# Kernel optimization log

Hardware: AMD Instinct MI355X
Metric: run time of the kernel (lower is better)

Reference implementation:

```python
import jax, jax.numpy as jnp
import numpy as np
import math

B, N, C_IN = 4, 512, 32
K = 3            # Chebyshev order -> K+1 polynomial terms
H = 4            # attention heads
OUT_PER_HEAD = 64
ACT_OUT = OUT_PER_HEAD * H  # concat_heads=True


def _prelu(x, a):
    return jnp.where(x >= 0, x, a * x)


def setup_inputs() -> dict:
    key = jax.random.key(0)
    ks = jax.random.split(key, 10)
    stdv = 1.0 / math.sqrt(ACT_OUT)
    inp = {
        "X_real": jax.random.normal(ks[0], (B, N, C_IN), jnp.float32),
        "X_imag": jax.random.normal(ks[1], (B, N, C_IN), jnp.float32),
        "L_real": jax.random.normal(ks[2], (B, K + 1, N, N), jnp.float32),
        "L_imag": jax.random.normal(ks[3], (B, K + 1, N, N), jnp.float32),
        # Chebyshev complex weights, uniform(-stdv, stdv) as in torch init
        "weight_real": jax.random.uniform(ks[4], (K + 1, C_IN, ACT_OUT), jnp.float32, -stdv, stdv),
        "weight_imag": jax.random.uniform(ks[5], (K + 1, C_IN, ACT_OUT), jnp.float32, -stdv, stdv),
        # CVLinear(2*C_IN -> H) complex weight/bias
        "attn_w_real": jax.random.normal(ks[6], (2 * C_IN, H), jnp.float32) * 0.1,
        "attn_w_imag": jax.random.normal(ks[7], (2 * C_IN, H), jnp.float32) * 0.1,
        "attn_b_real": jnp.zeros((H,), jnp.float32),
        "attn_b_imag": jnp.zeros((H,), jnp.float32),
        # CPReLU slopes (PReLU applied to real/imag parts independently)
        "prelu_a_real": jnp.float32(0.25),
        "prelu_a_imag": jnp.float32(0.25),
        "bias_real": jnp.zeros((1, ACT_OUT), jnp.float32),
        "bias_imag": jnp.zeros((1, ACT_OUT), jnp.float32),
    }
    return inp


def reference(X_real, X_imag, L_real, L_imag, weight_real, weight_imag,
              attn_w_real, attn_w_imag, attn_b_real, attn_b_imag,
              prelu_a_real, prelu_a_imag, bias_real, bias_imag):
    C = X_real.shape[-1]
    K1 = weight_real.shape[0]
    # --- attention scores: complex linear on concat([X_i, X_j]) ---
    # split the 2C weight into the X_i half and the X_j half (same math,
    # avoids materializing the B*N*N*2C pairwise concat tensor)
    W1r, W2r = attn_w_real[:C], attn_w_real[C:]
    W1i, W2i = attn_w_imag[:C], attn_w_imag[C:]
    si_re = X_real @ W1r - X_imag @ W1i   # (B,N,H)
    si_im = X_real @ W1i + X_imag @ W1r
    sj_re = X_real @ W2r - X_imag @ W2i
    sj_im = X_real @ W2i + X_imag @ W2r
    # scores[b,i,j,h]
    sc_re = si_re[:, :, None, :] + sj_re[:, None, :, :] + attn_b_real
    sc_im = si_im[:, :, None, :] + sj_im[:, None, :, :] + attn_b_imag
    # CPReLU: PReLU on real/imag independently
    sc_re = _prelu(sc_re, prelu_a_real)
    sc_im = _prelu(sc_im, prelu_a_imag)
    # adjacency mask from |L_real| summed over the K+1 polynomial terms
    mask = (jnp.abs(L_real).sum(axis=1) > 1e-9)[..., None]  # (B,N,N,1)
    NEG = jnp.float32(-1e9)
    re_m = jnp.where(mask, sc_re, NEG)
    im_m = jnp.where(mask, sc_im, NEG)
    attn = jax.nn.softmax(re_m * re_m + im_m * im_m, axis=2)  # softmax over j, (B,N,N,H)
    # --- complex Chebyshev propagation: (L*attn) @ X, per k, per head ---
    lre_xr = jnp.einsum('bknj,bnjh,bjc->bknch', L_real, attn, X_real)
    lim_xi = jnp.einsum('bknj,bnjh,bjc->bknch', L_imag, attn, X_imag)
    lre_xi = jnp.einsum('bknj,bnjh,bjc->bknch', L_real, attn, X_imag)
    lim_xr = jnp.einsum('bknj,bnjh,bjc->bknch', L_imag, attn, X_real)
    LXr = lre_xr - lim_xi
    LXi = lre_xi + lim_xr
    # per-head complex weights: (K+1, C, P, H), out index = p*H + h
    Wr = weight_real.reshape(K1, C, OUT_PER_HEAD, H)
    Wi = weight_imag.reshape(K1, C, OUT_PER_HEAD, H)
    Yre = jnp.einsum('bknch,kcph->bnph', LXr, Wr) - jnp.einsum('bknch,kcph->bnph', LXi, Wi)
    Yim = jnp.einsum('bknch,kcph->bnph', LXr, Wi) + jnp.einsum('bknch,kcph->bnph', LXi, Wr)
    Bsz, Nn = X_real.shape[:2]
    out_re = Yre.reshape(Bsz, Nn, -1) + bias_real
    out_im = Yim.reshape(Bsz, Nn, -1) + bias_imag
    return (out_re, out_im)
```

## Files before the change

### kernel.cpp

```cpp
#include <hip/hip_runtime.h>
#include <hip/hip_bf16.h>

#define BB 4
#define NN 512
#define CC 32
#define KK 4
#define HH 4
#define AOUT 256

#define WS_SI_F   0
#define WS_SII_F  (BB*NN*HH)
#define WS_SJR_F  (2*BB*NN*HH)
#define WS_SJI_F  (3*BB*NN*HH)
#define XT_BASE   131072
#define LX_BASE   393216
#define BRE_BASE  4587520
#define BIM_BASE  4718592

typedef __attribute__((ext_vector_type(8))) short bf16x8;
typedef __attribute__((ext_vector_type(4))) float f32x4;

__device__ __forceinline__ ushort f2bfu(float f){
    union { __hip_bfloat16 h; ushort u; } cv;
    cv.h = __float2bfloat16(f);
    return cv.u;
}
__device__ __forceinline__ short f2bfs(float f){ return (short)f2bfu(f); }
__device__ __forceinline__ float bfu2f(unsigned int u){ return __uint_as_float(u << 16); }

__global__ __launch_bounds__(256) void prep_kernel(
    const float* __restrict__ Xr, const float* __restrict__ Xi,
    const float* __restrict__ AWr, const float* __restrict__ AWi,
    const float* __restrict__ Wr, const float* __restrict__ Wi,
    float* __restrict__ ws, char* __restrict__ wsB)
{
    const int blk = blockIdx.x;
    const int t = threadIdx.x;

    if (blk < 32) {
        const int row = blk*64 + (t >> 2);
        const int q = t & 3;
        const float* xr = Xr + (size_t)row*CC + q*8;
        const float* xi = Xi + (size_t)row*CC + q*8;
        float4 xr4[2], xi4[2];
        xr4[0] = *(const float4*)xr;  xr4[1] = *(const float4*)(xr + 4);
        xi4[0] = *(const float4*)xi;  xi4[1] = *(const float4*)(xi + 4);

        float sir[HH] = {0,0,0,0}, sii[HH] = {0,0,0,0};
        float sjr[HH] = {0,0,0,0}, sji[HH] = {0,0,0,0};
        #pragma unroll
        for (int e = 0; e < 8; ++e) {
            float xrc = ((const float*)&xr4[e>>2])[e & 3];
            float xic = ((const float*)&xi4[e>>2])[e & 3];
            int c = q*8 + e;
            float4 w1r = *(const float4*)(AWr + c*HH);
            float4 w1i = *(const float4*)(AWi + c*HH);
            float4 w2r = *(const float4*)(AWr + (CC + c)*HH);
            float4 w2i = *(const float4*)(AWi + (CC + c)*HH);
            #pragma unroll
            for (int h = 0; h < HH; ++h) {
                float r1 = ((const float*)&w1r)[h], i1 = ((const float*)&w1i)[h];
                float r2 = ((const float*)&w2r)[h], i2 = ((const float*)&w2i)[h];
                sir[h] = fmaf(xrc, r1, fmaf(-xic, i1, sir[h]));
                sii[h] = fmaf(xrc, i1, fmaf( xic, r1, sii[h]));
                sjr[h] = fmaf(xrc, r2, fmaf(-xic, i2, sjr[h]));
                sji[h] = fmaf(xrc, i2, fmaf( xic, r2, sji[h]));
            }
        }
        float A[HH], Bv[HH];
        #pragma unroll
        for (int h = 0; h < HH; ++h) {
            float sendA = (q & 1) ? sir[h] : sii[h];
            float keepA = (q & 1) ? sii[h] : sir[h];
            A[h] = keepA + __shfl_xor(sendA, 1);
            float sendB = (q & 1) ? sjr[h] : sji[h];
            float keepB = (q & 1) ? sji[h] : sjr[h];
            Bv[h] = keepB + __shfl_xor(sendB, 1);
        }
        float tot[HH];
        #pragma unroll
        for (int h = 0; h < HH; ++h) {
            float send = (q & 2) ? A[h] : Bv[h];
            float keep = (q & 2) ? Bv[h] : A[h];
            tot[h] = keep + __shfl_xor(send, 2);
        }
        float4 v = make_float4(tot[0], tot[1], tot[2], tot[3]);
        *(float4*)(ws + (size_t)q*(BB*NN*HH) + (size_t)row*HH) = v;
    } else if (blk < 64) {
        int bid = (blk - 32)*4 + (t >> 6);
        int part = bid >> 6, b = (bid >> 4) & 3, jb = bid & 15;
        const float* X = part ? Xi : Xr;
        int lane = t & 63;
        int c = lane & 31, jh = lane >> 5;

        unsigned int w[8];
        #pragma unroll
        for (int qq = 0; qq < 8; ++qq) {
            int ji = jh*16 + qq*2;
            float f0 = X[((size_t)b*NN + jb*32 + ji  )*CC + c];
            float f1 = X[((size_t)b*NN + jb*32 + ji+1)*CC + c];
            w[qq] = (unsigned int)f2bfu(f0) | ((unsigned int)f2bfu(f1) << 16);
        }
        char* tile = wsB + XT_BASE + (((size_t)(part*4 + b)*16 + jb) * 2048);
        uint4* dst = (uint4*)(tile + c*64 + jh*32);
        dst[0] = make_uint4(w[0], w[1], w[2], w[3]);
        dst[1] = make_uint4(w[4], w[5], w[6], w[7]);
    } else {
        int idx = (blk - 64)*256 + t;
        int l  = idx & 63;
        int s  = (idx >> 6) & 7;
        int Nt = (idx >> 9) & 3;
        int h  = idx >> 11;
        int p = Nt*16 + (l & 15), o = p*4 + h;
        int e8 = (l >> 4) * 8;
        unsigned int re_w[4], im_w[4];
        #pragma unroll
        for (int qq = 0; qq < 4; ++qq) {
            unsigned int rw = 0, iw = 0;
            #pragma unroll
            for (int half = 0; half < 2; ++half) {
                int kpos = s*32 + e8 + qq*2 + half;
                int ri = kpos >> 7, kk = (kpos >> 5) & 3, c = kpos & 31;
                float wr = Wr[(size_t)(kk*CC + c)*AOUT + o];
                float wi = Wi[(size_t)(kk*CC + c)*AOUT + o];
                unsigned int vre = f2bfu(ri ? -wi : wr);
                unsigned int vim = f2bfu(ri ?  wr : wi);
                rw |= vre << (16*half);
                iw |= vim << (16*half);
            }
            re_w[qq] = rw; im_w[qq] = iw;
        }
        size_t fo = ((size_t)((h*4 + Nt)*8 + s))*1024 + (size_t)l*16;
        *(uint4*)(wsB + BRE_BASE + fo) = make_uint4(re_w[0], re_w[1], re_w[2], re_w[3]);
        *(uint4*)(wsB + BIM_BASE + fo) = make_uint4(im_w[0], im_w[1], im_w[2], im_w[3]);
    }
}

__global__ __launch_bounds__(128, 4) void cheb_main_kernel(
    const float* __restrict__ Lr_g, const float* __restrict__ Li_g,
    const float* __restrict__ abr, const float* __restrict__ abi,
    const float* __restrict__ par, const float* __restrict__ pai,
    const float* __restrict__ ws, char* __restrict__ wsB)
{
    __shared__ ushort Lf[8][528];
    __shared__ float awf[HH][520];
    __shared__ float wredm[2][HH];
    __shared__ float wreds[2][HH];

    const int bn = blockIdx.x;
    const int b = bn >> 9;
    const int n = bn & (NN - 1);
    const int t = threadIdx.x;
    const int l = t & 63;
    const int w = t >> 6;
    const int jw = 4*t;

    const float4 si_r4 = *(const float4*)(ws + WS_SI_F  + bn*HH);
    const float4 si_i4 = *(const float4*)(ws + WS_SII_F + bn*HH);
    float4 sjr[4], sji[4];
    #pragma unroll
    for (int e = 0; e < 4; ++e) {
        sjr[e] = *(const float4*)(ws + WS_SJR_F + ((size_t)b*NN + jw + e)*HH);
        sji[e] = *(const float4*)(ws + WS_SJI_F + ((size_t)b*NN + jw + e)*HH);
    }
    const float a_r = par[0], a_i = pai[0];

    const char* xtR = wsB + XT_BASE + ((size_t)(0*4 + b)*16 + w*8)*2048;
    const char* xtI = wsB + XT_BASE + ((size_t)(4   + b)*16 + w*8)*2048;
    const int jg  = l >> 4;
    const int bofs = (l & 15)*64 + jg*16;

#define LB(s, BR0,BR1,BI0,BI1) do {                                           \
        BR0 = *(const bf16x8*)(xtR + (s)*2048 +        bofs);                 \
        BR1 = *(const bf16x8*)(xtR + (s)*2048 + 1024 + bofs);                 \
        BI0 = *(const bf16x8*)(xtI + (s)*2048 +        bofs);                 \
        BI1 = *(const bf16x8*)(xtI + (s)*2048 + 1024 + bofs);                 \
    } while (0)

    bf16x8 pR0,pR1,pI0,pI1, qR0,qR1,qI0,qI1, rR0,rR1,rI0,rI1;
    LB(0, pR0,pR1,pI0,pI1);
    LB(1, qR0,qR1,qI0,qI1);

    float am4[4] = {0.f,0.f,0.f,0.f};
    #pragma unroll
    for (int it = 0; it < 8; ++it) {
        const float* src = (it & 4) ? Li_g : Lr_g;
        size_t goff = (((size_t)b*KK + (it & 3))*NN + n)*NN + jw;
        float4 v = *(const float4*)(src + goff);
        if (it < 4) {
            am4[0] += fabsf(v.x); am4[1] += fabsf(v.y);
            am4[2] += fabsf(v.z); am4[3] += fabsf(v.w);
        }
        ushort4 u;
        u.x = f2bfu(v.x); u.y = f2bfu(v.y); u.z = f2bfu(v.z); u.w = f2bfu(v.w);
        *(ushort4*)&Lf[it][jw] = u;
    }

    float sir[HH], sii[HH];
    #pragma unroll
    for (int h = 0; h < HH; ++h) {
        sir[h] = ((const float*)&si_r4)[h] + abr[h];
        sii[h] = ((const float*)&si_i4)[h] + abi[h];
    }
    float v[4][HH];
    float pmax[HH] = {-INFINITY, -INFINITY, -INFINITY, -INFINITY};
    #pragma unroll
    for (int e = 0; e < 4; ++e) {
        bool msk = am4[e] > 1e-9f;
        const float* sjrp = (const float*)&sjr[e];
        const float* sjip = (const float*)&sji[e];
        #pragma unroll
        for (int h = 0; h < HH; ++h) {
            float sr = sir[h] + sjrp[h];
            sr = sr >= 0.f ? sr : a_r * sr;
            float sv = sii[h] + sjip[h];
            sv = sv >= 0.f ? sv : a_i * sv;
            float val;
            if (msk) val = sr*sr + sv*sv;
            else { const float NEG = -1e9f; val = NEG*NEG + NEG*NEG; }
            v[e][h] = val;
            pmax[h] = fmaxf(pmax[h], val);
        }
    }
    #pragma unroll
    for (int h = 0; h < HH; ++h) {
        #pragma unroll
        for (int off = 32; off > 0; off >>= 1)
            pmax[h] = fmaxf(pmax[h], __shfl_xor(pmax[h], off));
    }
    if (l == 0) { wredm[w][0]=pmax[0]; wredm[w][1]=pmax[1]; wredm[w][2]=pmax[2]; wredm[w][3]=pmax[3]; }
    __syncthreads();

    float hm[HH];
    #pragma unroll
    for (int h = 0; h < HH; ++h) hm[h] = fmaxf(wredm[0][h], wredm[1][h]);

    float psum[HH];
    #pragma unroll
    for (int h = 0; h < HH; ++h) {
        float4 ev;
        ev.x = __expf(v[0][h] - hm[h]);
        ev.y = __expf(v[1][h] - hm[h]);
        ev.z = __expf(v[2][h] - hm[h]);
        ev.w = __expf(v[3][h] - hm[h]);
        *(float4*)&awf[h][jw] = ev;
        psum[h] = (ev.x + ev.y) + (ev.z + ev.w);
    }
    #pragma unroll
    for (int h = 0; h < HH; ++h) {
        #pragma unroll
        for (int off = 32; off > 0; off >>= 1)
            psum[h] += __shfl_xor(psum[h], off);
    }
    if (l == 0) { wreds[w][0]=psum[0]; wreds[w][1]=psum[1]; wreds[w][2]=psum[2]; wreds[w][3]=psum[3]; }
    __syncthreads();

    float inv[HH];
    #pragma unroll
    for (int h = 0; h < HH; ++h) inv[h] = 1.0f / (wreds[0][h] + wreds[1][h]);

    const int r_a = l & 15;
    const int k_a = r_a >> 2, h_a = r_a & 3;

    f32x4 acc[8];
    #pragma unroll
    for (int a = 0; a < 8; ++a) acc[a] = (f32x4){0.f,0.f,0.f,0.f};

#define COMP(s, BR0,BR1,BI0,BI1) do {                                         \
        const int j0_ = w*256 + (s)*32 + jg*8;                                \
        bf16x8 LR8 = *(const bf16x8*)&Lf[k_a][j0_];                           \
        bf16x8 LI8 = *(const bf16x8*)&Lf[4 + k_a][j0_];                       \
        float aww_[8];                                                        \
        *(float4*)&aww_[0] = *(const float4*)&awf[h_a][j0_];                  \
        *(float4*)&aww_[4] = *(const float4*)&awf[h_a][j0_ + 4];              \
        bf16x8 Ar_, Ai_;                                                      \
        _Pragma("unroll")                                                     \
        for (int e_ = 0; e_ < 8; ++e_) {                                      \
            Ar_[e_] = f2bfs(bfu2f((ushort)LR8[e_]) * aww_[e_]);               \
            Ai_[e_] = f2bfs(bfu2f((ushort)LI8[e_]) * aww_[e_]);               \
        }                                                                     \
        acc[0] = __builtin_amdgcn_mfma_f32_16x16x32_bf16(Ar_, BR0, acc[0],0,0,0); \
        acc[1] = __builtin_amdgcn_mfma_f32_16x16x32_bf16(Ar_, BR1, acc[1],0,0,0); \
        acc[2] = __builtin_amdgcn_mfma_f32_16x16x32_bf16(Ai_, BI0, acc[2],0,0,0); \
        acc[3] = __builtin_amdgcn_mfma_f32_16x16x32_bf16(Ai_, BI1, acc[3],0,0,0); \
        acc[4] = __builtin_amdgcn_mfma_f32_16x16x32_bf16(Ar_, BI0, acc[4],0,0,0); \
        acc[5] = __builtin_amdgcn_mfma_f32_16x16x32_bf16(Ar_, BI1, acc[5],0,0,0); \
        acc[6] = __builtin_amdgcn_mfma_f32_16x16x32_bf16(Ai_, BR0, acc[6],0,0,0); \
        acc[7] = __builtin_amdgcn_mfma_f32_16x16x32_bf16(Ai_, BR1, acc[7],0,0,0); \
    } while (0)

    LB(2, rR0,rR1,rI0,rI1);  COMP(0, pR0,pR1,pI0,pI1);
    LB(3, pR0,pR1,pI0,pI1);  COMP(1, qR0,qR1,qI0,qI1);
    LB(4, qR0,qR1,qI0,qI1);  COMP(2, rR0,rR1,rI0,rI1);
    LB(5, rR0,rR1,rI0,rI1);  COMP(3, pR0,pR1,pI0,pI1);
    LB(6, pR0,pR1,pI0,pI1);  COMP(4, qR0,qR1,qI0,qI1);
    LB(7, qR0,qR1,qI0,qI1);  COMP(5, rR0,rR1,rI0,rI1);
    COMP(6, pR0,pR1,pI0,pI1);
    COMP(7, qR0,qR1,qI0,qI1);
#undef LB
#undef COMP

    __syncthreads();

    float* pbuf = &awf[0][0];
    if (w == 1) {
        #pragma unroll
        for (int ae = 0; ae < 4; ++ae)
            #pragma unroll
            for (int r = 0; r < 4; ++r)
                pbuf[(ae*4 + r)*64 + l] = acc[2*ae][r];
    } else {
        #pragma unroll
        for (int ao = 0; ao < 4; ++ao)
            #pragma unroll
            for (int r = 0; r < 4; ++r)
                pbuf[1024 + (ao*4 + r)*64 + l] = acc[2*ao + 1][r];
    }
    __syncthreads();

    const int kk = l >> 4, lc = l & 15;
    char* lxp = wsB + LX_BASE + (size_t)bn*2048;
    if (w == 0) {
        #pragma unroll
        for (int ae = 0; ae < 4; ++ae)
            #pragma unroll
            for (int r = 0; r < 4; ++r)
                acc[2*ae][r] += pbuf[(ae*4 + r)*64 + l];
        #pragma unroll
        for (int r = 0; r < 4; ++r) {
            float iv = inv[r];
            float vr = (acc[0][r] - acc[2][r]) * iv;
            float vi = (acc[4][r] + acc[6][r]) * iv;
            *(ushort*)(lxp + r*512 +       kk*64 + lc*2) = f2bfu(vr);
            *(ushort*)(lxp + r*512 + 256 + kk*64 + lc*2) = f2bfu(vi);
        }
    } else {
        #pragma unroll
        for (int ao = 0; ao < 4; ++ao)
            #pragma unroll
            for (int r = 0; r < 4; ++r)
                acc[2*ao + 1][r] += pbuf[1024 + (ao*4 + r)*64 + l];
        const int c = 16 + lc;
        #pragma unroll
        for (int r = 0; r < 4; ++r) {
            float iv = inv[r];
            float vr = (acc[1][r] - acc[3][r]) * iv;
            float vi = (acc[5][r] + acc[7][r]) * iv;
            *(ushort*)(lxp + r*512 +       kk*64 + c*2) = f2bfu(vr);
            *(ushort*)(lxp + r*512 + 256 + kk*64 + c*2) = f2bfu(vi);
        }
    }
}

__global__ __launch_bounds__(256) void out_gemm_kernel(
    const char* __restrict__ wsB,
    const float* __restrict__ bsr, const float* __restrict__ bsi,
    float* __restrict__ out)
{
    const int Mtile = blockIdx.x >> 2;
    const int Nt    = blockIdx.x & 3;
    const int t = threadIdx.x, l = t & 63, h = t >> 6;

    const char* abase = wsB + LX_BASE + ((size_t)(Mtile*16 + (l & 15)))*2048
                        + h*512 + (l >> 4)*16;
    f32x4 are = (f32x4){0.f,0.f,0.f,0.f};
    f32x4 aim = (f32x4){0.f,0.f,0.f,0.f};
    const size_t fbase = ((size_t)((h*4 + Nt)*8))*1024 + (size_t)l*16;
    const char* bre = wsB + BRE_BASE + fbase;
    const char* bim = wsB + BIM_BASE + fbase;
    #pragma unroll
    for (int s = 0; s < 8; ++s) {
        bf16x8 Af = *(const bf16x8*)(abase + s*64);
        bf16x8 Br = *(const bf16x8*)(bre + s*1024);
        bf16x8 Bi = *(const bf16x8*)(bim + s*1024);
        are = __builtin_amdgcn_mfma_f32_16x16x32_bf16(Af, Br, are, 0, 0, 0);
        aim = __builtin_amdgcn_mfma_f32_16x16x32_bf16(Af, Bi, aim, 0, 0, 0);
    }
    const int p = Nt*16 + (l & 15), o = p*4 + h;
    const float vbr = bsr[o], vbi = bsi[o];
    #pragma unroll
    for (int r = 0; r < 4; ++r) {
        int bn = Mtile*16 + (l >> 4)*4 + r;
        out[(size_t)bn*AOUT + o] = are[r] + vbr;
        out[(size_t)BB*NN*AOUT + (size_t)bn*AOUT + o] = aim[r] + vbi;
    }
}

extern "C" void kernel_launch(void* const* d_in, const int* in_sizes, int n_in,
                              void* d_out, int out_size, void* d_ws, size_t ws_size,
                              hipStream_t stream)
{
    const float* Xr  = (const float*)d_in[0];
    const float* Xi  = (const float*)d_in[1];
    const float* Lr  = (const float*)d_in[2];
    const float* Li  = (const float*)d_in[3];
    const float* Wr  = (const float*)d_in[4];
    const float* Wi  = (const float*)d_in[5];
    const float* AWr = (const float*)d_in[6];
    const float* AWi = (const float*)d_in[7];
    const float* abr = (const float*)d_in[8];
    const float* abi = (const float*)d_in[9];
    const float* par = (const float*)d_in[10];
    const float* pai = (const float*)d_in[11];
    const float* bsr = (const float*)d_in[12];
    const float* bsi = (const float*)d_in[13];
    float* ws  = (float*)d_ws;
    char*  wsB = (char*)d_ws;
    float* out = (float*)d_out;

    hipLaunchKernelGGL(prep_kernel, dim3(96), dim3(256), 0, stream,
                       Xr, Xi, AWr, AWi, Wr, Wi, ws, wsB);
    hipLaunchKernelGGL(cheb_main_kernel, dim3(BB*NN), dim3(128), 0, stream,
                       Lr, Li, abr, abi, par, pai, ws, wsB);
    hipLaunchKernelGGL(out_gemm_kernel, dim3(512), dim3(256), 0, stream,
                       wsB, bsr, bsi, out);
}
```

Baseline: 32.84 us.

## Use four waves per row in cheb main kernel with tree reduction

Raises the cheb_main_kernel block from 128 to 256 threads, so each wave covers 128 columns of j instead of 256. The L loads are split between real and imaginary halves, with the mask row-sums shared through LDS, and the MFMA partial sums are combined across four waves in a two-stage LDS reduction. The goal is more memory-level parallelism and a shorter per-wave MFMA chain. In exchange it adds extra barriers and reduction traffic, and the deeper software prefetch of X tiles is dropped.

```diff
diff --git a/kernel.cpp b/kernel.cpp
--- a/kernel.cpp
+++ b/kernel.cpp
@@ -136,7 +136,7 @@
     }
 }
 
-__global__ __launch_bounds__(128, 4) void cheb_main_kernel(
+__global__ __launch_bounds__(256) void cheb_main_kernel(
     const float* __restrict__ Lr_g, const float* __restrict__ Li_g,
     const float* __restrict__ abr, const float* __restrict__ abi,
     const float* __restrict__ par, const float* __restrict__ pai,
@@ -144,8 +144,9 @@
 {
     __shared__ ushort Lf[8][528];
     __shared__ float awf[HH][520];
-    __shared__ float wredm[2][HH];
-    __shared__ float wreds[2][HH];
+    __shared__ float amb[512];
+    __shared__ float wredm[4][HH];
+    __shared__ float wreds[4][HH];
 
     const int bn = blockIdx.x;
     const int b = bn >> 9;
@@ -153,20 +154,20 @@
     const int t = threadIdx.x;
     const int l = t & 63;
     const int w = t >> 6;
-    const int jw = 4*t;
+    const int jw2 = 2*t;
 
     const float4 si_r4 = *(const float4*)(ws + WS_SI_F  + bn*HH);
     const float4 si_i4 = *(const float4*)(ws + WS_SII_F + bn*HH);
-    float4 sjr[4], sji[4];
-    #pragma unroll
-    for (int e = 0; e < 4; ++e) {
-        sjr[e] = *(const float4*)(ws + WS_SJR_F + ((size_t)b*NN + jw + e)*HH);
-        sji[e] = *(const float4*)(ws + WS_SJI_F + ((size_t)b*NN + jw + e)*HH);
+    float4 sjr[2], sji[2];
+    #pragma unroll
+    for (int e = 0; e < 2; ++e) {
+        sjr[e] = *(const float4*)(ws + WS_SJR_F + ((size_t)b*NN + jw2 + e)*HH);
+        sji[e] = *(const float4*)(ws + WS_SJI_F + ((size_t)b*NN + jw2 + e)*HH);
     }
     const float a_r = par[0], a_i = pai[0];
 
-    const char* xtR = wsB + XT_BASE + ((size_t)(0*4 + b)*16 + w*8)*2048;
-    const char* xtI = wsB + XT_BASE + ((size_t)(4   + b)*16 + w*8)*2048;
+    const char* xtR = wsB + XT_BASE + ((size_t)(0*4 + b)*16 + w*4)*2048;
+    const char* xtI = wsB + XT_BASE + ((size_t)(4   + b)*16 + w*4)*2048;
     const int jg  = l >> 4;
     const int bofs = (l & 15)*64 + jg*16;
 
@@ -177,23 +178,28 @@
         BI1 = *(const bf16x8*)(xtI + (s)*2048 + 1024 + bofs);                 \
     } while (0)
 
-    bf16x8 pR0,pR1,pI0,pI1, qR0,qR1,qI0,qI1, rR0,rR1,rI0,rI1;
+    bf16x8 pR0,pR1,pI0,pI1, qR0,qR1,qI0,qI1;
     LB(0, pR0,pR1,pI0,pI1);
     LB(1, qR0,qR1,qI0,qI1);
 
-    float am4[4] = {0.f,0.f,0.f,0.f};
-    #pragma unroll
-    for (int it = 0; it < 8; ++it) {
-        const float* src = (it & 4) ? Li_g : Lr_g;
-        size_t goff = (((size_t)b*KK + (it & 3))*NN + n)*NN + jw;
-        float4 v = *(const float4*)(src + goff);
-        if (it < 4) {
-            am4[0] += fabsf(v.x); am4[1] += fabsf(v.y);
-            am4[2] += fabsf(v.z); am4[3] += fabsf(v.w);
-        }
-        ushort4 u;
-        u.x = f2bfu(v.x); u.y = f2bfu(v.y); u.z = f2bfu(v.z); u.w = f2bfu(v.w);
-        *(ushort4*)&Lf[it][jw] = u;
+    {
+        const int half = t >> 7;
+        const int jc = (t & 127) * 4;
+        const float* src = half ? Li_g : Lr_g;
+        float am4[4] = {0.f,0.f,0.f,0.f};
+        #pragma unroll
+        for (int it = 0; it < 4; ++it) {
+            size_t goff = (((size_t)b*KK + it)*NN + n)*NN + jc;
+            float4 v = *(const float4*)(src + goff);
+            if (half == 0) {
+                am4[0] += fabsf(v.x); am4[1] += fabsf(v.y);
+                am4[2] += fabsf(v.z); am4[3] += fabsf(v.w);
+            }
+            ushort4 u;
+            u.x = f2bfu(v.x); u.y = f2bfu(v.y); u.z = f2bfu(v.z); u.w = f2bfu(v.w);
+            *(ushort4*)&Lf[half*4 + it][jc] = u;
+        }
+        if (half == 0) *(float4*)&amb[jc] = *(float4*)am4;
     }
 
     float sir[HH], sii[HH];
@@ -202,11 +208,9 @@
         sir[h] = ((const float*)&si_r4)[h] + abr[h];
         sii[h] = ((const float*)&si_i4)[h] + abi[h];
     }
-    float v[4][HH];
-    float pmax[HH] = {-INFINITY, -INFINITY, -INFINITY, -INFINITY};
-    #pragma unroll
-    for (int e = 0; e < 4; ++e) {
-        bool msk = am4[e] > 1e-9f;
+    float v[2][HH];
+    #pragma unroll
+    for (int e = 0; e < 2; ++e) {
         const float* sjrp = (const float*)&sjr[e];
         const float* sjip = (const float*)&sji[e];
         #pragma unroll
@@ -215,15 +219,26 @@
             sr = sr >= 0.f ? sr : a_r * sr;
             float sv = sii[h] + sjip[h];
             sv = sv >= 0.f ? sv : a_i * sv;
-            float val;
-            if (msk) val = sr*sr + sv*sv;
-            else { const float NEG = -1e9f; val = NEG*NEG + NEG*NEG; }
-            v[e][h] = val;
-            pmax[h] = fmaxf(pmax[h], val);
-        }
-    }
+            v[e][h] = sr*sr + sv*sv;
+        }
+    }
+    __syncthreads();
+
+    {
+        const float NEG = -1e9f;
+        const float MASKED = NEG*NEG + NEG*NEG;
+        float a0 = amb[jw2], a1 = amb[jw2 + 1];
+        bool m0 = a0 > 1e-9f, m1 = a1 > 1e-9f;
+        #pragma unroll
+        for (int h = 0; h < HH; ++h) {
+            v[0][h] = m0 ? v[0][h] : MASKED;
+            v[1][h] = m1 ? v[1][h] : MASKED;
+        }
+    }
+    float pmax[HH];
     #pragma unroll
     for (int h = 0; h < HH; ++h) {
+        pmax[h] = fmaxf(v[0][h], v[1][h]);
         #pragma unroll
         for (int off = 32; off > 0; off >>= 1)
             pmax[h] = fmaxf(pmax[h], __shfl_xor(pmax[h], off));
@@ -233,21 +248,17 @@
 
     float hm[HH];
     #pragma unroll
-    for (int h = 0; h < HH; ++h) hm[h] = fmaxf(wredm[0][h], wredm[1][h]);
+    for (int h = 0; h < HH; ++h)
+        hm[h] = fmaxf(fmaxf(wredm[0][h], wredm[1][h]), fmaxf(wredm[2][h], wredm[3][h]));
 
     float psum[HH];
     #pragma unroll
     for (int h = 0; h < HH; ++h) {
-        float4 ev;
-        ev.x = __expf(v[0][h] - hm[h]);
-        ev.y = __expf(v[1][h] - hm[h]);
-        ev.z = __expf(v[2][h] - hm[h]);
-        ev.w = __expf(v[3][h] - hm[h]);
-        *(float4*)&awf[h][jw] = ev;
-        psum[h] = (ev.x + ev.y) + (ev.z + ev.w);
-    }
-    #pragma unroll
-    for (int h = 0; h < HH; ++h) {
+        float e0 = __expf(v[0][h] - hm[h]);
+        float e1 = __expf(v[1][h] - hm[h]);
+        float2 ev = make_float2(e0, e1);
+        *(float2*)&awf[h][jw2] = ev;
+        psum[h] = e0 + e1;
         #pragma unroll
         for (int off = 32; off > 0; off >>= 1)
             psum[h] += __shfl_xor(psum[h], off);
@@ -257,7 +268,8 @@
 
     float inv[HH];
     #pragma unroll
-    for (int h = 0; h < HH; ++h) inv[h] = 1.0f / (wreds[0][h] + wreds[1][h]);
+    for (int h = 0; h < HH; ++h)
+        inv[h] = 1.0f / (((wreds[0][h] + wreds[1][h]) + (wreds[2][h] + wreds[3][h])));
 
     const int r_a = l & 15;
     const int k_a = r_a >> 2, h_a = r_a & 3;
@@ -267,7 +279,7 @@
     for (int a = 0; a < 8; ++a) acc[a] = (f32x4){0.f,0.f,0.f,0.f};
 
 #define COMP(s, BR0,BR1,BI0,BI1) do {                                         \
-        const int j0_ = w*256 + (s)*32 + jg*8;                                \
+        const int j0_ = w*128 + (s)*32 + jg*8;                                \
         bf16x8 LR8 = *(const bf16x8*)&Lf[k_a][j0_];                           \
         bf16x8 LI8 = *(const bf16x8*)&Lf[4 + k_a][j0_];                       \
         float aww_[8];                                                        \
@@ -289,32 +301,55 @@
         acc[7] = __builtin_amdgcn_mfma_f32_16x16x32_bf16(Ai_, BR1, acc[7],0,0,0); \
     } while (0)
 
-    LB(2, rR0,rR1,rI0,rI1);  COMP(0, pR0,pR1,pI0,pI1);
-    LB(3, pR0,pR1,pI0,pI1);  COMP(1, qR0,qR1,qI0,qI1);
-    LB(4, qR0,qR1,qI0,qI1);  COMP(2, rR0,rR1,rI0,rI1);
-    LB(5, rR0,rR1,rI0,rI1);  COMP(3, pR0,pR1,pI0,pI1);
-    LB(6, pR0,pR1,pI0,pI1);  COMP(4, qR0,qR1,qI0,qI1);
-    LB(7, qR0,qR1,qI0,qI1);  COMP(5, rR0,rR1,rI0,rI1);
-    COMP(6, pR0,pR1,pI0,pI1);
-    COMP(7, qR0,qR1,qI0,qI1);
+    COMP(0, pR0,pR1,pI0,pI1);
+    LB(2, pR0,pR1,pI0,pI1);
+    COMP(1, qR0,qR1,qI0,qI1);
+    LB(3, qR0,qR1,qI0,qI1);
+    COMP(2, pR0,pR1,pI0,pI1);
+    COMP(3, qR0,qR1,qI0,qI1);
 #undef LB
 #undef COMP
 
     __syncthreads();
 
-    float* pbuf = &awf[0][0];
+    float* pbufA = &awf[0][0];
+    float* pbufB = (float*)&Lf[0][0];
     if (w == 1) {
         #pragma unroll
+        for (int a = 0; a < 8; ++a)
+            #pragma unroll
+            for (int r = 0; r < 4; ++r)
+                pbufA[(a*4 + r)*64 + l] = acc[a][r];
+    } else if (w == 3) {
+        #pragma unroll
+        for (int a = 0; a < 8; ++a)
+            #pragma unroll
+            for (int r = 0; r < 4; ++r)
+                pbufB[(a*4 + r)*64 + l] = acc[a][r];
+    }
+    __syncthreads();
+    if (w == 0) {
+        #pragma unroll
+        for (int a = 0; a < 8; ++a)
+            #pragma unroll
+            for (int r = 0; r < 4; ++r)
+                acc[a][r] += pbufA[(a*4 + r)*64 + l];
+        #pragma unroll
+        for (int ao = 0; ao < 4; ++ao)
+            #pragma unroll
+            for (int r = 0; r < 4; ++r)
+                pbufB[1024 + (ao*4 + r)*64 + l] = acc[2*ao + 1][r];
+    } else if (w == 2) {
+        #pragma unroll
+        for (int a = 0; a < 8; ++a)
+            #pragma unroll
+            for (int r = 0; r < 4; ++r)
+                acc[a][r] += pbufB[(a*4 + r)*64 + l];
+        #pragma unroll
         for (int ae = 0; ae < 4; ++ae)
             #pragma unroll
             for (int r = 0; r < 4; ++r)
-                pbuf[(ae*4 + r)*64 + l] = acc[2*ae][r];
-    } else {
-        #pragma unroll
-        for (int ao = 0; ao < 4; ++ao)
-            #pragma unroll
-            for (int r = 0; r < 4; ++r)
-                pbuf[1024 + (ao*4 + r)*64 + l] = acc[2*ao + 1][r];
+                pbufA[(ae*4 + r)*64 + l] = acc[2*ae][r];
     }
     __syncthreads();
 
@@ -325,7 +360,7 @@
         for (int ae = 0; ae < 4; ++ae)
             #pragma unroll
             for (int r = 0; r < 4; ++r)
-                acc[2*ae][r] += pbuf[(ae*4 + r)*64 + l];
+                acc[2*ae][r] += pbufA[(ae*4 + r)*64 + l];
         #pragma unroll
         for (int r = 0; r < 4; ++r) {
             float iv = inv[r];
@@ -334,12 +369,12 @@
             *(ushort*)(lxp + r*512 +       kk*64 + lc*2) = f2bfu(vr);
             *(ushort*)(lxp + r*512 + 256 + kk*64 + lc*2) = f2bfu(vi);
         }
-    } else {
+    } else if (w == 2) {
         #pragma unroll
         for (int ao = 0; ao < 4; ++ao)
             #pragma unroll
             for (int r = 0; r < 4; ++r)
-                acc[2*ao + 1][r] += pbuf[1024 + (ao*4 + r)*64 + l];
+                acc[2*ao + 1][r] += pbufB[1024 + (ao*4 + r)*64 + l];
         const int c = 16 + lc;
         #pragma unroll
         for (int r = 0; r < 4; ++r) {
@@ -410,7 +445,7 @@
 
     hipLaunchKernelGGL(prep_kernel, dim3(96), dim3(256), 0, stream,
                        Xr, Xi, AWr, AWi, Wr, Wi, ws, wsB);
-    hipLaunchKernelGGL(cheb_main_kernel, dim3(BB*NN), dim3(128), 0, stream,
+    hipLaunchKernelGGL(cheb_main_kernel, dim3(BB*NN), dim3(256), 0, stream,
                        Lr, Li, abr, abi, par, pai, ws, wsB);
     hipLaunchKernelGGL(out_gemm_kernel, dim3(512), dim3(256), 0, stream,
                        wsB, bsr, bsi, out);
```

Result: slower. 37.02 us (+12.7%).

## Process two graph nodes per block to reuse X tiles across MFMA work

Applied to the files above, without the earlier changes.

Each cheb_main block now handles two consecutive nodes n0 and n0+1 instead of one, halving the grid. The bf16 X operand loads and the sj score loads are shared between both nodes, and all 16 L loads are issued up front. The softmax of the second node is interleaved with the first node's reduction to hide sync latency. This doubles accumulator and shared-memory footprint and drops the occupancy hint from launch bounds, so fewer waves fit per CU and register pressure rises. The X prefetch depth also shrinks from three buffers to two.

```diff
diff --git a/kernel.cpp b/kernel.cpp
--- a/kernel.cpp
+++ b/kernel.cpp
@@ -136,27 +136,30 @@
     }
 }
 
-__global__ __launch_bounds__(128, 4) void cheb_main_kernel(
+__global__ __launch_bounds__(128) void cheb_main_kernel(
     const float* __restrict__ Lr_g, const float* __restrict__ Li_g,
     const float* __restrict__ abr, const float* __restrict__ abi,
     const float* __restrict__ par, const float* __restrict__ pai,
     const float* __restrict__ ws, char* __restrict__ wsB)
 {
-    __shared__ ushort Lf[8][528];
-    __shared__ float awf[HH][520];
-    __shared__ float wredm[2][HH];
-    __shared__ float wreds[2][HH];
-
-    const int bn = blockIdx.x;
-    const int b = bn >> 9;
-    const int n = bn & (NN - 1);
+    __shared__ ushort Lf[2][8][528];
+    __shared__ float awf[2][HH][520];
+    __shared__ float wredm[2][2][HH];
+    __shared__ float wreds[2][2][HH];
+
+    const int blk = blockIdx.x;
+    const int b = blk >> 8;
+    const int n0 = (blk & 255) * 2;
+    const int bn0 = b*NN + n0;
     const int t = threadIdx.x;
     const int l = t & 63;
     const int w = t >> 6;
     const int jw = 4*t;
 
-    const float4 si_r4 = *(const float4*)(ws + WS_SI_F  + bn*HH);
-    const float4 si_i4 = *(const float4*)(ws + WS_SII_F + bn*HH);
+    const float4 si_r0 = *(const float4*)(ws + WS_SI_F  + (size_t)bn0*HH);
+    const float4 si_i0 = *(const float4*)(ws + WS_SII_F + (size_t)bn0*HH);
+    const float4 si_r1 = *(const float4*)(ws + WS_SI_F  + (size_t)(bn0+1)*HH);
+    const float4 si_i1 = *(const float4*)(ws + WS_SII_F + (size_t)(bn0+1)*HH);
     float4 sjr[4], sji[4];
     #pragma unroll
     for (int e = 0; e < 4; ++e) {
@@ -164,6 +167,68 @@
         sji[e] = *(const float4*)(ws + WS_SJI_F + ((size_t)b*NN + jw + e)*HH);
     }
     const float a_r = par[0], a_i = pai[0];
+
+    float4 v0[8], v1[8];
+    #pragma unroll
+    for (int it = 0; it < 8; ++it) {
+        const float* src = (it & 4) ? Li_g : Lr_g;
+        size_t goff = (((size_t)b*KK + (it & 3))*NN + n0)*NN + jw;
+        v0[it] = *(const float4*)(src + goff);
+    }
+    #pragma unroll
+    for (int it = 0; it < 8; ++it) {
+        const float* src = (it & 4) ? Li_g : Lr_g;
+        size_t goff = (((size_t)b*KK + (it & 3))*NN + (n0+1))*NN + jw;
+        v1[it] = *(const float4*)(src + goff);
+    }
+
+    float am0[4] = {0.f,0.f,0.f,0.f};
+    #pragma unroll
+    for (int it = 0; it < 8; ++it) {
+        float4 v = v0[it];
+        if (it < 4) {
+            am0[0] += fabsf(v.x); am0[1] += fabsf(v.y);
+            am0[2] += fabsf(v.z); am0[3] += fabsf(v.w);
+        }
+        ushort4 u;
+        u.x = f2bfu(v.x); u.y = f2bfu(v.y); u.z = f2bfu(v.z); u.w = f2bfu(v.w);
+        *(ushort4*)&Lf[0][it][jw] = u;
+    }
+
+    float sir0[HH], sii0[HH];
+    #pragma unroll
+    for (int h = 0; h < HH; ++h) {
+        sir0[h] = ((const float*)&si_r0)[h] + abr[h];
+        sii0[h] = ((const float*)&si_i0)[h] + abi[h];
+    }
+    float sc0[4][HH];
+    float pmax0[HH] = {-INFINITY, -INFINITY, -INFINITY, -INFINITY};
+    #pragma unroll
+    for (int e = 0; e < 4; ++e) {
+        bool msk = am0[e] > 1e-9f;
+        const float* sjrp = (const float*)&sjr[e];
+        const float* sjip = (const float*)&sji[e];
+        #pragma unroll
+        for (int h = 0; h < HH; ++h) {
+            float sr = sir0[h] + sjrp[h];
+            sr = sr >= 0.f ? sr : a_r * sr;
+            float sv = sii0[h] + sjip[h];
+            sv = sv >= 0.f ? sv : a_i * sv;
+            float val;
+            if (msk) val = sr*sr + sv*sv;
+            else { const float NEG = -1e9f; val = NEG*NEG + NEG*NEG; }
+            sc0[e][h] = val;
+            pmax0[h] = fmaxf(pmax0[h], val);
+        }
+    }
+    #pragma unroll
+    for (int h = 0; h < HH; ++h) {
+        #pragma unroll
+        for (int off = 32; off > 0; off >>= 1)
+            pmax0[h] = fmaxf(pmax0[h], __shfl_xor(pmax0[h], off));
+    }
+    if (l == 0) { wredm[0][w][0]=pmax0[0]; wredm[0][w][1]=pmax0[1]; wredm[0][w][2]=pmax0[2]; wredm[0][w][3]=pmax0[3]; }
+    __syncthreads();
 
     const char* xtR = wsB + XT_BASE + ((size_t)(0*4 + b)*16 + w*8)*2048;
     const char* xtI = wsB + XT_BASE + ((size_t)(4   + b)*16 + w*8)*2048;
@@ -177,124 +242,160 @@
         BI1 = *(const bf16x8*)(xtI + (s)*2048 + 1024 + bofs);                 \
     } while (0)
 
-    bf16x8 pR0,pR1,pI0,pI1, qR0,qR1,qI0,qI1, rR0,rR1,rI0,rI1;
+    bf16x8 pR0,pR1,pI0,pI1, qR0,qR1,qI0,qI1;
     LB(0, pR0,pR1,pI0,pI1);
     LB(1, qR0,qR1,qI0,qI1);
 
-    float am4[4] = {0.f,0.f,0.f,0.f};
+    float hm0[HH];
+    #pragma unroll
+    for (int h = 0; h < HH; ++h) hm0[h] = fmaxf(wredm[0][0][h], wredm[0][1][h]);
+    float psum0[HH];
+    #pragma unroll
+    for (int h = 0; h < HH; ++h) {
+        float4 ev;
+        ev.x = __expf(sc0[0][h] - hm0[h]);
+        ev.y = __expf(sc0[1][h] - hm0[h]);
+        ev.z = __expf(sc0[2][h] - hm0[h]);
+        ev.w = __expf(sc0[3][h] - hm0[h]);
+        *(float4*)&awf[0][h][jw] = ev;
+        psum0[h] = (ev.x + ev.y) + (ev.z + ev.w);
+        #pragma unroll
+        for (int off = 32; off > 0; off >>= 1)
+            psum0[h] += __shfl_xor(psum0[h], off);
+    }
+    if (l == 0) { wreds[0][w][0]=psum0[0]; wreds[0][w][1]=psum0[1]; wreds[0][w][2]=psum0[2]; wreds[0][w][3]=psum0[3]; }
+
+    float am1[4] = {0.f,0.f,0.f,0.f};
     #pragma unroll
     for (int it = 0; it < 8; ++it) {
-        const float* src = (it & 4) ? Li_g : Lr_g;
-        size_t goff = (((size_t)b*KK + (it & 3))*NN + n)*NN + jw;
-        float4 v = *(const float4*)(src + goff);
+        float4 v = v1[it];
         if (it < 4) {
-            am4[0] += fabsf(v.x); am4[1] += fabsf(v.y);
-            am4[2] += fabsf(v.z); am4[3] += fabsf(v.w);
+            am1[0] += fabsf(v.x); am1[1] += fabsf(v.y);
+            am1[2] += fabsf(v.z); am1[3] += fabsf(v.w);
         }
         ushort4 u;
         u.x = f2bfu(v.x); u.y = f2bfu(v.y); u.z = f2bfu(v.z); u.w = f2bfu(v.w);
-        *(ushort4*)&Lf[it][jw] = u;
-    }
-
-    float sir[HH], sii[HH];
+        *(ushort4*)&Lf[1][it][jw] = u;
+    }
+    float sir1[HH], sii1[HH];
     #pragma unroll
     for (int h = 0; h < HH; ++h) {
-        sir[h] = ((const float*)&si_r4)[h] + abr[h];
-        sii[h] = ((const float*)&si_i4)[h] + abi[h];
-    }
-    float v[4][HH];
-    float pmax[HH] = {-INFINITY, -INFINITY, -INFINITY, -INFINITY};
+        sir1[h] = ((const float*)&si_r1)[h] + abr[h];
+        sii1[h] = ((const float*)&si_i1)[h] + abi[h];
+    }
+    float sc1[4][HH];
+    float pmax1[HH] = {-INFINITY, -INFINITY, -INFINITY, -INFINITY};
     #pragma unroll
     for (int e = 0; e < 4; ++e) {
-        bool msk = am4[e] > 1e-9f;
+        bool msk = am1[e] > 1e-9f;
         const float* sjrp = (const float*)&sjr[e];
         const float* sjip = (const float*)&sji[e];
         #pragma unroll
         for (int h = 0; h < HH; ++h) {
-            float sr = sir[h] + sjrp[h];
+            float sr = sir1[h] + sjrp[h];
             sr = sr >= 0.f ? sr : a_r * sr;
-            float sv = sii[h] + sjip[h];
+            float sv = sii1[h] + sjip[h];
             sv = sv >= 0.f ? sv : a_i * sv;
             float val;
             if (msk) val = sr*sr + sv*sv;
             else { const float NEG = -1e9f; val = NEG*NEG + NEG*NEG; }
-            v[e][h] = val;
-            pmax[h] = fmaxf(pmax[h], val);
+            sc1[e][h] = val;
+            pmax1[h] = fmaxf(pmax1[h], val);
         }
     }
     #pragma unroll
     for (int h = 0; h < HH; ++h) {
         #pragma unroll
         for (int off = 32; off > 0; off >>= 1)
-            pmax[h] = fmaxf(pmax[h], __shfl_xor(pmax[h], off));
-    }
-    if (l == 0) { wredm[w][0]=pmax[0]; wredm[w][1]=pmax[1]; wredm[w][2]=pmax[2]; wredm[w][3]=pmax[3]; }
+            pmax1[h] = fmaxf(pmax1[h], __shfl_xor(pmax1[h], off));
+    }
+    if (l == 0) { wredm[1][w][0]=pmax1[0]; wredm[1][w][1]=pmax1[1]; wredm[1][w][2]=pmax1[2]; wredm[1][w][3]=pmax1[3]; }
     __syncthreads();
 
-    float hm[HH];
-    #pragma unroll
-    for (int h = 0; h < HH; ++h) hm[h] = fmaxf(wredm[0][h], wredm[1][h]);
-
-    float psum[HH];
+    float inv0[HH];
+    #pragma unroll
+    for (int h = 0; h < HH; ++h) inv0[h] = 1.0f / (wreds[0][0][h] + wreds[0][1][h]);
+
+    float hm1[HH];
+    #pragma unroll
+    for (int h = 0; h < HH; ++h) hm1[h] = fmaxf(wredm[1][0][h], wredm[1][1][h]);
+    float psum1[HH];
     #pragma unroll
     for (int h = 0; h < HH; ++h) {
         float4 ev;
-        ev.x = __expf(v[0][h] - hm[h]);
-        ev.y = __expf(v[1][h] - hm[h]);
-        ev.z = __expf(v[2][h] - hm[h]);
-        ev.w = __expf(v[3][h] - hm[h]);
-        *(float4*)&awf[h][jw] = ev;
-        psum[h] = (ev.x + ev.y) + (ev.z + ev.w);
-    }
-    #pragma unroll
-    for (int h = 0; h < HH; ++h) {
+        ev.x = __expf(sc1[0][h] - hm1[h]);
+        ev.y = __expf(sc1[1][h] - hm1[h]);
+        ev.z = __expf(sc1[2][h] - hm1[h]);
+        ev.w = __expf(sc1[3][h] - hm1[h]);
+        *(float4*)&awf[1][h][jw] = ev;
+        psum1[h] = (ev.x + ev.y) + (ev.z + ev.w);
         #pragma unroll
         for (int off = 32; off > 0; off >>= 1)
-            psum[h] += __shfl_xor(psum[h], off);
-    }
-    if (l == 0) { wreds[w][0]=psum[0]; wreds[w][1]=psum[1]; wreds[w][2]=psum[2]; wreds[w][3]=psum[3]; }
+            psum1[h] += __shfl_xor(psum1[h], off);
+    }
+    if (l == 0) { wreds[1][w][0]=psum1[0]; wreds[1][w][1]=psum1[1]; wreds[1][w][2]=psum1[2]; wreds[1][w][3]=psum1[3]; }
     __syncthreads();
 
-    float inv[HH];
-    #pragma unroll
-    for (int h = 0; h < HH; ++h) inv[h] = 1.0f / (wreds[0][h] + wreds[1][h]);
+    float inv1[HH];
+    #pragma unroll
+    for (int h = 0; h < HH; ++h) inv1[h] = 1.0f / (wreds[1][0][h] + wreds[1][1][h]);
 
     const int r_a = l & 15;
     const int k_a = r_a >> 2, h_a = r_a & 3;
 
-    f32x4 acc[8];
-    #pragma unroll
-    for (int a = 0; a < 8; ++a) acc[a] = (f32x4){0.f,0.f,0.f,0.f};
+    f32x4 acc0[8], acc1[8];
+    #pragma unroll
+    for (int a = 0; a < 8; ++a) { acc0[a] = (f32x4){0.f,0.f,0.f,0.f}; acc1[a] = (f32x4){0.f,0.f,0.f,0.f}; }
 
 #define COMP(s, BR0,BR1,BI0,BI1) do {                                         \
         const int j0_ = w*256 + (s)*32 + jg*8;                                \
-        bf16x8 LR8 = *(const bf16x8*)&Lf[k_a][j0_];                           \
-        bf16x8 LI8 = *(const bf16x8*)&Lf[4 + k_a][j0_];                       \
-        float aww_[8];                                                        \
-        *(float4*)&aww_[0] = *(const float4*)&awf[h_a][j0_];                  \
-        *(float4*)&aww_[4] = *(const float4*)&awf[h_a][j0_ + 4];              \
-        bf16x8 Ar_, Ai_;                                                      \
+        bf16x8 LR0 = *(const bf16x8*)&Lf[0][k_a][j0_];                        \
+        bf16x8 LI0 = *(const bf16x8*)&Lf[0][4 + k_a][j0_];                    \
+        bf16x8 LR1 = *(const bf16x8*)&Lf[1][k_a][j0_];                        \
+        bf16x8 LI1 = *(const bf16x8*)&Lf[1][4 + k_a][j0_];                    \
+        float aw0_[8], aw1_[8];                                               \
+        *(float4*)&aw0_[0] = *(const float4*)&awf[0][h_a][j0_];               \
+        *(float4*)&aw0_[4] = *(const float4*)&awf[0][h_a][j0_ + 4];           \
+        *(float4*)&aw1_[0] = *(const float4*)&awf[1][h_a][j0_];               \
+        *(float4*)&aw1_[4] = *(const float4*)&awf[1][h_a][j0_ + 4];           \
+        bf16x8 Ar0_, Ai0_, Ar1_, Ai1_;                                        \
         _Pragma("unroll")                                                     \
         for (int e_ = 0; e_ < 8; ++e_) {                                      \
-            Ar_[e_] = f2bfs(bfu2f((ushort)LR8[e_]) * aww_[e_]);               \
-            Ai_[e_] = f2bfs(bfu2f((ushort)LI8[e_]) * aww_[e_]);               \
+            Ar0_[e_] = f2bfs(bfu2f((ushort)LR0[e_]) * aw0_[e_]);              \
+            Ai0_[e_] = f2bfs(bfu2f((ushort)LI0[e_]) * aw0_[e_]);              \
+            Ar1_[e_] = f2bfs(bfu2f((ushort)LR1[e_]) * aw1_[e_]);              \
+            Ai1_[e_] = f2bfs(bfu2f((ushort)LI1[e_]) * aw1_[e_]);              \
         }                                                                     \
-        acc[0] = __builtin_amdgcn_mfma_f32_16x16x32_bf16(Ar_, BR0, acc[0],0,0,0); \
-        acc[1] = __builtin_amdgcn_mfma_f32_16x16x32_bf16(Ar_, BR1, acc[1],0,0,0); \
-        acc[2] = __builtin_amdgcn_mfma_f32_16x16x32_bf16(Ai_, BI0, acc[2],0,0,0); \
-        acc[3] = __builtin_amdgcn_mfma_f32_16x16x32_bf16(Ai_, BI1, acc[3],0,0,0); \
-        acc[4] = __builtin_amdgcn_mfma_f32_16x16x32_bf16(Ar_, BI0, acc[4],0,0,0); \
-        acc[5] = __builtin_amdgcn_mfma_f32_16x16x32_bf16(Ar_, BI1, acc[5],0,0,0); \
-        acc[6] = __builtin_amdgcn_mfma_f32_16x16x32_bf16(Ai_, BR0, acc[6],0,0,0); \
-        acc[7] = __builtin_amdgcn_mfma_f32_16x16x32_bf16(Ai_, BR1, acc[7],0,0,0); \
+        acc0[0] = __builtin_amdgcn_mfma_f32_16x16x32_bf16(Ar0_, BR0, acc0[0],0,0,0); \
+        acc0[1] = __builtin_amdgcn_mfma_f32_16x16x32_bf16(Ar0_, BR1, acc0[1],0,0,0); \
+        acc0[2] = __builtin_amdgcn_mfma_f32_16x16x32_bf16(Ai0_, BI0, acc0[2],0,0,0); \
+        acc0[3] = __builtin_amdgcn_mfma_f32_16x16x32_bf16(Ai0_, BI1, acc0[3],0,0,0); \
+        acc0[4] = __builtin_amdgcn_mfma_f32_16x16x32_bf16(Ar0_, BI0, acc0[4],0,0,0); \
+        acc0[5] = __builtin_amdgcn_mfma_f32_16x16x32_bf16(Ar0_, BI1, acc0[5],0,0,0); \
+        acc0[6] = __builtin_amdgcn_mfma_f32_16x16x32_bf16(Ai0_, BR0, acc0[6],0,0,0); \
+        acc0[7] = __builtin_amdgcn_mfma_f32_16x16x32_bf16(Ai0_, BR1, acc0[7],0,0,0); \
+        acc1[0] = __builtin_amdgcn_mfma_f32_16x16x32_bf16(Ar1_, BR0, acc1[0],0,0,0); \
+        acc1[1] = __builtin_amdgcn_mfma_f32_16x16x32_bf16(Ar1_, BR1, acc1[1],0,0,0); \
+        acc1[2] = __builtin_amdgcn_mfma_f32_16x16x32_bf16(Ai1_, BI0, acc1[2],0,0,0); \
+        acc1[3] = __builtin_amdgcn_mfma_f32_16x16x32_bf16(Ai1_, BI1, acc1[3],0,0,0); \
+        acc1[4] = __builtin_amdgcn_mfma_f32_16x16x32_bf16(Ar1_, BI0, acc1[4],0,0,0); \
+        acc1[5] = __builtin_amdgcn_mfma_f32_16x16x32_bf16(Ar1_, BI1, acc1[5],0,0,0); \
+        acc1[6] = __builtin_amdgcn_mfma_f32_16x16x32_bf16(Ai1_, BR0, acc1[6],0,0,0); \
+        acc1[7] = __builtin_amdgcn_mfma_f32_16x16x32_bf16(Ai1_, BR1, acc1[7],0,0,0); \
     } while (0)
 
-    LB(2, rR0,rR1,rI0,rI1);  COMP(0, pR0,pR1,pI0,pI1);
-    LB(3, pR0,pR1,pI0,pI1);  COMP(1, qR0,qR1,qI0,qI1);
-    LB(4, qR0,qR1,qI0,qI1);  COMP(2, rR0,rR1,rI0,rI1);
-    LB(5, rR0,rR1,rI0,rI1);  COMP(3, pR0,pR1,pI0,pI1);
-    LB(6, pR0,pR1,pI0,pI1);  COMP(4, qR0,qR1,qI0,qI1);
-    LB(7, qR0,qR1,qI0,qI1);  COMP(5, rR0,rR1,rI0,rI1);
+    COMP(0, pR0,pR1,pI0,pI1);
+    LB(2, pR0,pR1,pI0,pI1);
+    COMP(1, qR0,qR1,qI0,qI1);
+    LB(3, qR0,qR1,qI0,qI1);
+    COMP(2, pR0,pR1,pI0,pI1);
+    LB(4, pR0,pR1,pI0,pI1);
+    COMP(3, qR0,qR1,qI0,qI1);
+    LB(5, qR0,qR1,qI0,qI1);
+    COMP(4, pR0,pR1,pI0,pI1);
+    LB(6, pR0,pR1,pI0,pI1);
+    COMP(5, qR0,qR1,qI0,qI1);
+    LB(7, qR0,qR1,qI0,qI1);
     COMP(6, pR0,pR1,pI0,pI1);
     COMP(7, qR0,qR1,qI0,qI1);
 #undef LB
@@ -302,52 +403,62 @@
 
     __syncthreads();
 
-    float* pbuf = &awf[0][0];
+    float* pbuf0 = &awf[0][0][0];
+    float* pbuf1 = &awf[1][0][0];
     if (w == 1) {
         #pragma unroll
         for (int ae = 0; ae < 4; ++ae)
             #pragma unroll
-            for (int r = 0; r < 4; ++r)
-                pbuf[(ae*4 + r)*64 + l] = acc[2*ae][r];
+            for (int r = 0; r < 4; ++r) {
+                pbuf0[(ae*4 + r)*64 + l] = acc0[2*ae][r];
+                pbuf1[(ae*4 + r)*64 + l] = acc1[2*ae][r];
+            }
     } else {
         #pragma unroll
         for (int ao = 0; ao < 4; ++ao)
             #pragma unroll
-            for (int r = 0; r < 4; ++r)
-                pbuf[1024 + (ao*4 + r)*64 + l] = acc[2*ao + 1][r];
+            for (int r = 0; r < 4; ++r) {
+                pbuf0[1024 + (ao*4 + r)*64 + l] = acc0[2*ao + 1][r];
+                pbuf1[1024 + (ao*4 + r)*64 + l] = acc1[2*ao + 1][r];
+            }
     }
     __syncthreads();
 
     const int kk = l >> 4, lc = l & 15;
-    char* lxp = wsB + LX_BASE + (size_t)bn*2048;
+    char* lxp0 = wsB + LX_BASE + (size_t)bn0*2048;
+    char* lxp1 = lxp0 + 2048;
     if (w == 0) {
         #pragma unroll
         for (int ae = 0; ae < 4; ++ae)
             #pragma unroll
-            for (int r = 0; r < 4; ++r)
-                acc[2*ae][r] += pbuf[(ae*4 + r)*64 + l];
+            for (int r = 0; r < 4; ++r) {
+                acc0[2*ae][r] += pbuf0[(ae*4 + r)*64 + l];
+                acc1[2*ae][r] += pbuf1[(ae*4 + r)*64 + l];
+            }
         #pragma unroll
         for (int r = 0; r < 4; ++r) {
-            float iv = inv[r];
-            float vr = (acc[0][r] - acc[2][r]) * iv;
-            float vi = (acc[4][r] + acc[6][r]) * iv;
-            *(ushort*)(lxp + r*512 +       kk*64 + lc*2) = f2bfu(vr);
-            *(ushort*)(lxp + r*512 + 256 + kk*64 + lc*2) = f2bfu(vi);
+            float iv0 = inv0[r], iv1 = inv1[r];
+            *(ushort*)(lxp0 + r*512 +       kk*64 + lc*2) = f2bfu((acc0[0][r] - acc0[2][r]) * iv0);
+            *(ushort*)(lxp0 + r*512 + 256 + kk*64 + lc*2) = f2bfu((acc0[4][r] + acc0[6][r]) * iv0);
+            *(ushort*)(lxp1 + r*512 +       kk*64 + lc*2) = f2bfu((acc1[0][r] - acc1[2][r]) * iv1);
+            *(ushort*)(lxp1 + r*512 + 256 + kk*64 + lc*2) = f2bfu((acc1[4][r] + acc1[6][r]) * iv1);
         }
     } else {
         #pragma unroll
         for (int ao = 0; ao < 4; ++ao)
             #pragma unroll
-            for (int r = 0; r < 4; ++r)
-                acc[2*ao + 1][r] += pbuf[1024 + (ao*4 + r)*64 + l];
+            for (int r = 0; r < 4; ++r) {
+                acc0[2*ao + 1][r] += pbuf0[1024 + (ao*4 + r)*64 + l];
+                acc1[2*ao + 1][r] += pbuf1[1024 + (ao*4 + r)*64 + l];
+            }
         const int c = 16 + lc;
         #pragma unroll
         for (int r = 0; r < 4; ++r) {
-            float iv = inv[r];
-            float vr = (acc[1][r] - acc[3][r]) * iv;
-            float vi = (acc[5][r] + acc[7][r]) * iv;
-            *(ushort*)(lxp + r*512 +       kk*64 + c*2) = f2bfu(vr);
-            *(ushort*)(lxp + r*512 + 256 + kk*64 + c*2) = f2bfu(vi);
+            float iv0 = inv0[r], iv1 = inv1[r];
+            *(ushort*)(lxp0 + r*512 +       kk*64 + c*2) = f2bfu((acc0[1][r] - acc0[3][r]) * iv0);
+            *(ushort*)(lxp0 + r*512 + 256 + kk*64 + c*2) = f2bfu((acc0[5][r] + acc0[7][r]) * iv0);
+            *(ushort*)(lxp1 + r*512 +       kk*64 + c*2) = f2bfu((acc1[1][r] - acc1[3][r]) * iv1);
+            *(ushort*)(lxp1 + r*512 + 256 + kk*64 + c*2) = f2bfu((acc1[5][r] + acc1[7][r]) * iv1);
         }
     }
 }
@@ -410,7 +521,7 @@
 
     hipLaunchKernelGGL(prep_kernel, dim3(96), dim3(256), 0, stream,
                        Xr, Xi, AWr, AWi, Wr, Wi, ws, wsB);
-    hipLaunchKernelGGL(cheb_main_kernel, dim3(BB*NN), dim3(128), 0, stream,
+    hipLaunchKernelGGL(cheb_main_kernel, dim3(BB*NN/2), dim3(128), 0, stream,
                        Lr, Li, abr, abi, par, pai, ws, wsB);
     hipLaunchKernelGGL(out_gemm_kernel, dim3(512), dim3(256), 0, stream,
                        wsB, bsr, bsi, out);
```

New measurement: 33.64 us. 2.4% more time.
